# Optimization experiments

Measured on AMD Instinct MI355X. Metric: run time of the kernel, lower is better.

## Reference

```python
import jax, jax.numpy as jnp
import numpy as np

N_QUBITS = 12
DIM = 1 << N_QUBITS
W_MUL = (2.0 ** 0.5) * (5.0 ** -0.5)  # he_std * lrmul with gain=sqrt(2), lrmul=1


def _pair_gates(thetas):
    """thetas: [P,3] angles (rxx, ryy, rzz) -> [P,4,4] gate Rzz@Ryy@Rxx per pair."""
    c = jnp.cos(thetas / 2).astype(jnp.complex64)
    s = jnp.sin(thetas / 2).astype(jnp.complex64)
    I4 = jnp.eye(4, dtype=jnp.complex64)
    X = jnp.array([[0, 1], [1, 0]], jnp.complex64)
    Y = jnp.array([[0, -1j], [1j, 0]], jnp.complex64)
    Z = jnp.array([[1, 0], [0, -1]], jnp.complex64)
    XX, YY, ZZ = jnp.kron(X, X), jnp.kron(Y, Y), jnp.kron(Z, Z)
    rot = lambda cc, ss, P: cc[:, None, None] * I4 - 1j * ss[:, None, None] * P
    Rxx = rot(c[:, 0], s[:, 0], XX)
    Ryy = rot(c[:, 1], s[:, 1], YY)
    Rzz = rot(c[:, 2], s[:, 2], ZZ)
    # circuit applies rxx, then ryy, then rzz -> U_pair = Rzz @ Ryy @ Rxx
    return jnp.einsum('pij,pjk,pkl->pil', Rzz, Ryy, Rxx)


def _build_U(weight):
    n = N_QUBITS
    w = weight * W_MUL
    # i = 3*n + 3*which_q for which_q in 0,2,...,n-2 (as in qconv0)
    idx = 3 * n + 3 * np.arange(0, n, 2)
    thetas = jnp.stack([w[idx], w[idx + 1], w[idx + 2]], axis=-1)  # [n/2, 3]
    G = _pair_gates(thetas)
    U = G[0]
    for p in range(1, n // 2):  # qubit 0 is the most-significant leg
        U = jnp.kron(U, G[p])
    return U  # [DIM, DIM]


def setup_inputs() -> dict:
    key = jax.random.key(0)
    kx, kw = jax.random.split(key)
    x = jax.random.normal(kx, (2, 1, DIM), dtype=jnp.float32)
    x = x / jnp.linalg.norm(x, axis=-1, keepdims=True)  # normalized quantum states
    weight = jax.random.uniform(kw, (6 * N_QUBITS,), dtype=jnp.float32,
                                minval=0.0, maxval=2 * np.pi)
    return {"x": x, "weight": weight, "dimA": N_QUBITS // 2}


def reference(x, weight, dimA):
    n, dim = N_QUBITS, DIM
    B = x.shape[0]
    psi = x.astype(jnp.complex64)[:, 0, :]                    # [B, dim]
    rho = jnp.einsum('bi,bj->bij', psi, jnp.conj(psi))        # rho = psi psi^dagger
    U = _build_U(weight)
    rho2 = jnp.einsum('ij,bjk,lk->bil', U, rho, jnp.conj(U))  # U rho U^dagger
    dimB = n - dimA
    dB, dA = 1 << dimB, 1 << dimA
    # partial trace over leading dimB qubits (trace_lst = range(dimB))
    red = jnp.einsum('btitj->bij', rho2.reshape(B, dB, dA, dB, dA))
    return red.reshape(B, 1, dA * dA)  # dA*dA == dim since dimA = n/2
```

## Files before the change

### kernel.cpp

```cpp
#include <hip/hip_runtime.h>

#define DIMQ 4096
#define NPAIR 6
#define DA 64

__device__ __forceinline__ float2 cmul(float2 a, float2 b) {
    return make_float2(a.x*b.x - a.y*b.y, a.x*b.y + a.y*b.x);
}
__device__ __forceinline__ float2 cfma2(float2 a, float2 u, float2 b, float2 v) {
    return make_float2(a.x*u.x - a.y*u.y + b.x*v.x - b.y*v.y,
                       a.x*u.y + a.y*u.x + b.x*v.y + b.y*v.x);
}

__global__ __launch_bounds__(1024) void quconv_kernel(
    const float* __restrict__ x,
    const float* __restrict__ w,
    float* __restrict__ out,
    int real_only)
{
    __shared__ float2 buf[DIMQ];
    __shared__ float2 G[NPAIR][4];

    const int tid = threadIdx.x;
    const int b   = blockIdx.x >> 4;
    const int s   = blockIdx.x & 15;

    if (tid < NPAIR) {
        const float WM = 0.63245553203367586640f;
        const int base = 36 + 6 * tid;
        const float tx = 0.5f * WM * w[base + 0];
        const float ty = 0.5f * WM * w[base + 1];
        const float tz = 0.5f * WM * w[base + 2];
        float cm, sm, cp, sp, cz, sz;
        __sincosf(tx - ty, &sm, &cm);
        __sincosf(tx + ty, &sp, &cp);
        __sincosf(tz,      &sz, &cz);
        const float2 em = make_float2(cz, -sz);
        const float2 ep = make_float2(cz,  sz);
        G[tid][0] = make_float2(cz * cm, -sz * cm);
        G[tid][1] = cmul(em, make_float2(0.f, -sm));
        G[tid][2] = make_float2(cz * cp,  sz * cp);
        G[tid][3] = cmul(ep, make_float2(0.f, -sp));
    }

    const float r0 = x[b * DIMQ + tid];
    const float r1 = x[b * DIMQ + tid + 1024];
    const float r2 = x[b * DIMQ + tid + 2048];
    const float r3 = x[b * DIMQ + tid + 3072];

    __syncthreads();

    {
        const float2 A = G[0][0], B = G[0][1], C = G[0][2], D = G[0][3];
        buf[tid]        = make_float2(A.x*r0 + B.x*r3, A.y*r0 + B.y*r3);
        buf[tid + 1024] = make_float2(C.x*r1 + D.x*r2, C.y*r1 + D.y*r2);
        buf[tid + 2048] = make_float2(D.x*r1 + C.x*r2, D.y*r1 + C.y*r2);
        buf[tid + 3072] = make_float2(B.x*r0 + A.x*r3, B.y*r0 + A.y*r3);
    }

    for (int p = 1; p < NPAIR; ++p) {
        __syncthreads();
        const int shift = 2 * (5 - p);
        const int g = tid;
        const int low  = g & ((1 << shift) - 1);
        const int base = ((g >> shift) << (shift + 2)) | low;
        const int s1 = 1 << shift;
        const float2 A = G[p][0], B = G[p][1], C = G[p][2], D = G[p][3];
        const float2 v0 = buf[base];
        const float2 v1 = buf[base + s1];
        const float2 v2 = buf[base + 2 * s1];
        const float2 v3 = buf[base + 3 * s1];
        buf[base]          = cfma2(A, v0, B, v3);
        buf[base + s1]     = cfma2(C, v1, D, v2);
        buf[base + 2 * s1] = cfma2(D, v1, C, v2);
        buf[base + 3 * s1] = cfma2(B, v0, A, v3);
    }
    __syncthreads();

    const int c = tid & 3;
    const int j = (tid >> 2) & 63;
    const int i = (s << 2) + (tid >> 8);
    float re = 0.f, im = 0.f;
    const int t0 = c << 4;
    #pragma unroll
    for (int t = t0; t < t0 + 16; ++t) {
        const float2 pi = buf[t * DA + i];
        const float2 pj = buf[t * DA + j];
        re += pi.x * pj.x + pi.y * pj.y;
        im += pi.y * pj.x - pi.x * pj.y;
    }
    re += __shfl_xor(re, 1); im += __shfl_xor(im, 1);
    re += __shfl_xor(re, 2); im += __shfl_xor(im, 2);
    if (c == 0) {
        const int e = b * (DA * DA) + i * DA + j;
        if (real_only) {
            out[e] = re;
        } else {
            ((float2*)out)[e] = make_float2(re, im);
        }
    }
}

extern "C" void kernel_launch(void* const* d_in, const int* in_sizes, int n_in,
                              void* d_out, int out_size, void* d_ws, size_t ws_size,
                              hipStream_t stream) {
    const float* x = (const float*)d_in[0];
    const float* w = (const float*)d_in[1];
    const int B = in_sizes[0] / DIMQ;
    const int real_only = (out_size == B * DA * DA) ? 1 : 0;
    quconv_kernel<<<dim3(B * 16), dim3(1024), 0, stream>>>(x, w, (float*)d_out, real_only);
}
```

Measured before the change: 62.41 us.

## Split reduced-density output one row per block and pad shared state buffer

The grid grows from 16 to 64 blocks per batch element, and each block now computes a single output row i instead of four. The partial-trace reduction is split 16 ways across threads and combined with extra shuffle steps. The shared state buffer gets one padding element per 64 entries to cut LDS bank conflicts in the gate stages and the strided reduction reads. The trade-off is that every block still recomputes the full 4096-element gate pipeline, so that redundant work grows fourfold.

```diff
diff --git a/kernel.cpp b/kernel.cpp
--- a/kernel.cpp
+++ b/kernel.cpp
@@ -3,6 +3,8 @@
 #define DIMQ 4096
 #define NPAIR 6
 #define DA 64
+
+#define PAD(i) ((i) + ((i) >> 6))
 
 __device__ __forceinline__ float2 cmul(float2 a, float2 b) {
     return make_float2(a.x*b.x - a.y*b.y, a.x*b.y + a.y*b.x);
@@ -18,12 +20,12 @@
     float* __restrict__ out,
     int real_only)
 {
-    __shared__ float2 buf[DIMQ];
+    __shared__ float2 buf[DIMQ + DIMQ / 64];
     __shared__ float2 G[NPAIR][4];
 
     const int tid = threadIdx.x;
-    const int b   = blockIdx.x >> 4;
-    const int s   = blockIdx.x & 15;
+    const int b   = blockIdx.x >> 6;
+    const int i   = blockIdx.x & 63;
 
     if (tid < NPAIR) {
         const float WM = 0.63245553203367586640f;
@@ -52,10 +54,10 @@
 
     {
         const float2 A = G[0][0], B = G[0][1], C = G[0][2], D = G[0][3];
-        buf[tid]        = make_float2(A.x*r0 + B.x*r3, A.y*r0 + B.y*r3);
-        buf[tid + 1024] = make_float2(C.x*r1 + D.x*r2, C.y*r1 + D.y*r2);
-        buf[tid + 2048] = make_float2(D.x*r1 + C.x*r2, D.y*r1 + C.y*r2);
-        buf[tid + 3072] = make_float2(B.x*r0 + A.x*r3, B.y*r0 + A.y*r3);
+        buf[PAD(tid)]        = make_float2(A.x*r0 + B.x*r3, A.y*r0 + B.y*r3);
+        buf[PAD(tid + 1024)] = make_float2(C.x*r1 + D.x*r2, C.y*r1 + D.y*r2);
+        buf[PAD(tid + 2048)] = make_float2(D.x*r1 + C.x*r2, D.y*r1 + C.y*r2);
+        buf[PAD(tid + 3072)] = make_float2(B.x*r0 + A.x*r3, B.y*r0 + A.y*r3);
     }
 
     for (int p = 1; p < NPAIR; ++p) {
@@ -65,32 +67,37 @@
         const int low  = g & ((1 << shift) - 1);
         const int base = ((g >> shift) << (shift + 2)) | low;
         const int s1 = 1 << shift;
+        const int e0 = PAD(base);
+        const int e1 = PAD(base + s1);
+        const int e2 = PAD(base + 2 * s1);
+        const int e3 = PAD(base + 3 * s1);
         const float2 A = G[p][0], B = G[p][1], C = G[p][2], D = G[p][3];
-        const float2 v0 = buf[base];
-        const float2 v1 = buf[base + s1];
-        const float2 v2 = buf[base + 2 * s1];
-        const float2 v3 = buf[base + 3 * s1];
-        buf[base]          = cfma2(A, v0, B, v3);
-        buf[base + s1]     = cfma2(C, v1, D, v2);
-        buf[base + 2 * s1] = cfma2(D, v1, C, v2);
-        buf[base + 3 * s1] = cfma2(B, v0, A, v3);
+        const float2 v0 = buf[e0];
+        const float2 v1 = buf[e1];
+        const float2 v2 = buf[e2];
+        const float2 v3 = buf[e3];
+        buf[e0] = cfma2(A, v0, B, v3);
+        buf[e1] = cfma2(C, v1, D, v2);
+        buf[e2] = cfma2(D, v1, C, v2);
+        buf[e3] = cfma2(B, v0, A, v3);
     }
     __syncthreads();
 
-    const int c = tid & 3;
-    const int j = (tid >> 2) & 63;
-    const int i = (s << 2) + (tid >> 8);
+    const int c = tid & 15;
+    const int j = tid >> 4;
     float re = 0.f, im = 0.f;
-    const int t0 = c << 4;
     #pragma unroll
-    for (int t = t0; t < t0 + 16; ++t) {
-        const float2 pi = buf[t * DA + i];
-        const float2 pj = buf[t * DA + j];
+    for (int k = 0; k < 4; ++k) {
+        const int t = (c << 2) + k;
+        const float2 pi = buf[t * (DA + 1) + i];
+        const float2 pj = buf[t * (DA + 1) + j];
         re += pi.x * pj.x + pi.y * pj.y;
         im += pi.y * pj.x - pi.x * pj.y;
     }
     re += __shfl_xor(re, 1); im += __shfl_xor(im, 1);
     re += __shfl_xor(re, 2); im += __shfl_xor(im, 2);
+    re += __shfl_xor(re, 4); im += __shfl_xor(im, 4);
+    re += __shfl_xor(re, 8); im += __shfl_xor(im, 8);
     if (c == 0) {
         const int e = b * (DA * DA) + i * DA + j;
         if (real_only) {
@@ -108,5 +115,5 @@
     const float* w = (const float*)d_in[1];
     const int B = in_sizes[0] / DIMQ;
     const int real_only = (out_size == B * DA * DA) ? 1 : 0;
-    quconv_kernel<<<dim3(B * 16), dim3(1024), 0, stream>>>(x, w, (float*)d_out, real_only);
+    quconv_kernel<<<dim3(B * 64), dim3(1024), 0, stream>>>(x, w, (float*)d_out, real_only);
 }
```

Measured after the change: 60.64 us. 2.8% less time.
